# Kernel tuning notes

Hardware: AMD Instinct MI355X
Metric: run time of the kernel (lower is better)

The kernel has to match this reference:

```python
import jax, jax.numpy as jnp
import numpy as np
from jax import lax

EPS = 1e-6
DT_RANK = 24  # ceil(384/16), Mamba convention
D_STATE = 16


def _ln(x, g, b, eps=EPS):
    m = jnp.mean(x, axis=-1, keepdims=True)
    v = jnp.mean((x - m) ** 2, axis=-1, keepdims=True)
    return (x - m) * lax.rsqrt(v + eps) * g + b


def setup_inputs() -> dict:
    key = jax.random.key(0)
    ks = jax.random.split(key, 10)
    B, Dd, Hh, Ww, C = 2, 8, 16, 16, 384
    di, ds, r = 384, D_STATE, DT_RANK  # d_inner = expand * d_model = 384
    s = 0.02
    f = lambda k, shape: (jax.random.normal(k, shape, jnp.float32) * s)
    return {
        "x": jax.random.normal(ks[0], (B, Dd, Hh, Ww, C), jnp.float32),
        "g1": jnp.ones((C,), jnp.float32), "b1": jnp.zeros((C,), jnp.float32),
        "W_in": f(ks[1], (C, 2 * di)), "b_in": jnp.zeros((2 * di,), jnp.float32),
        "conv_w": f(ks[2], (di, 1, 3, 3, 3)), "conv_b": jnp.zeros((di,), jnp.float32),
        "W_x": f(ks[3], (di, r + 2 * ds)),
        "W_dt": f(ks[4], (r, di)), "b_dt": jnp.zeros((di,), jnp.float32),
        "A_log": jnp.tile(jnp.log(jnp.arange(1, ds + 1, dtype=jnp.float32)), (di, 1)),
        "D_skip": jnp.ones((di,), jnp.float32),
        "on_g": jnp.ones((di,), jnp.float32), "on_b": jnp.zeros((di,), jnp.float32),
        "W_out": f(ks[5], (di, C)), "b_out": jnp.zeros((C,), jnp.float32),
        "g2": jnp.ones((C,), jnp.float32), "b2": jnp.zeros((C,), jnp.float32),
        "W1": f(ks[6], (C, C)), "b1m": jnp.zeros((C,), jnp.float32),
        "W2": f(ks[7], (C, C)), "b2m": jnp.zeros((C,), jnp.float32),
    }


def _ss3d(h, W_in, b_in, conv_w, conv_b, W_x, W_dt, b_dt, A_log, D_skip, on_g, on_b, W_out, b_out):
    # h: [B, D, H, W, C] -> Mamba-style selective scan over flattened DHW (orientation 0)
    B, Dd, Hh, Ww, C = h.shape
    di = W_in.shape[1] // 2
    ds = D_STATE
    L = Dd * Hh * Ww
    seq = h.reshape(B, L, C)
    xz = seq @ W_in + b_in                      # [B, L, 2*di]
    xin, z = jnp.split(xz, 2, axis=-1)
    # depthwise 3D conv + SiLU on the x branch
    xc = xin.reshape(B, Dd, Hh, Ww, di).transpose(0, 4, 1, 2, 3)  # [B, di, D, H, W]
    xc = lax.conv_general_dilated(xc, conv_w, (1, 1, 1), 'SAME',
                                  feature_group_count=di,
                                  dimension_numbers=('NCDHW', 'OIDHW', 'NCDHW'))
    xc = xc + conv_b[None, :, None, None, None]
    xin = jax.nn.silu(xc).transpose(0, 2, 3, 4, 1).reshape(B, L, di)
    # input-dependent dt, B, C
    dbc = xin @ W_x                              # [B, L, r + 2*ds]
    dt, Bm, Cm = jnp.split(dbc, [DT_RANK, DT_RANK + ds], axis=-1)
    dt = jax.nn.softplus(dt @ W_dt + b_dt)       # [B, L, di]
    A = -jnp.exp(A_log)                          # [di, ds]
    dA = jnp.exp(dt[..., None] * A)              # [B, L, di, ds]
    dBx = dt[..., None] * Bm[:, :, None, :] * xin[..., None]  # [B, L, di, ds]

    def step(carry, inp):
        da, dbx, c = inp                         # [B,di,ds], [B,di,ds], [B,ds]
        carry = da * carry + dbx
        y = jnp.einsum('bds,bs->bd', carry, c)
        return carry, y

    xs = (dA.transpose(1, 0, 2, 3), dBx.transpose(1, 0, 2, 3), Cm.transpose(1, 0, 2))
    h0 = jnp.zeros((B, di, ds), dA.dtype)
    _, ys = lax.scan(step, h0, xs)               # ys: [L, B, di]
    y = ys.transpose(1, 0, 2) + xin * D_skip
    y = _ln(y, on_g, on_b) * jax.nn.silu(z)
    out = y @ W_out + b_out
    return out.reshape(B, Dd, Hh, Ww, C)


def reference(x, g1, b1, W_in, b_in, conv_w, conv_b, W_x, W_dt, b_dt, A_log, D_skip,
              on_g, on_b, W_out, b_out, g2, b2, W1, b1m, W2, b2m):
    # x + SS3D(LN(x)); then x + MLP(LN(x)).  drop_path/dropout = 0 (eval)
    a = _ss3d(_ln(x, g1, b1), W_in, b_in, conv_w, conv_b, W_x, W_dt, b_dt,
              A_log, D_skip, on_g, on_b, W_out, b_out)
    x1 = x + a
    h2 = _ln(x1, g2, b2)
    mlp = jax.nn.gelu(h2 @ W1 + b1m) @ W2 + b2m
    return x1 + mlp
```

## Files before the change

kernel.cpp:

```cpp
#include <hip/hip_runtime.h>
#include <hip/hip_bf16.h>

using bf16 = __hip_bfloat16;
#define DEV __device__ __forceinline__

typedef __attribute__((ext_vector_type(8))) short short8;
typedef __attribute__((ext_vector_type(8))) unsigned short ushort8;
typedef __attribute__((ext_vector_type(4))) float f32x4;

constexpr int Bb = 2, DD = 8, HH = 16, WW = 16;
constexpr int C = 384, DI = 384, DS = 16, RR = 24;
constexpr int L = DD * HH * WW;
constexpr int M = Bb * L;

DEV bf16 f2b(float v) { return __float2bfloat16(v); }
DEV unsigned short f2bu(float v) {
    bf16 t = __float2bfloat16(v);
    unsigned short u; __builtin_memcpy(&u, &t, 2); return u;
}
DEV float braw(unsigned short u) {
    unsigned int x = ((unsigned int)u) << 16;
    float f; __builtin_memcpy(&f, &x, 4); return f;
}

DEV float wred64(float v) {
    #pragma unroll
    for (int off = 32; off > 0; off >>= 1) v += __shfl_xor(v, off, 64);
    return v;
}
DEV float siluf(float x) { return x / (1.0f + __expf(-x)); }
DEV float softplusf(float x) { return (x > 15.0f) ? x : log1pf(__expf(x)); }
DEV float gelu_tanh(float x) {
    const float k0 = 0.7978845608028654f;
    float u = k0 * (x + 0.044715f * x * x * x);
    float e = __expf(2.0f * u);
    float t = 1.0f - 2.0f / (e + 1.0f);
    return 0.5f * x * (1.0f + t);
}

__global__ void detect_k(const unsigned short* __restrict__ g1raw,
                         int* __restrict__ flag) {
    if (threadIdx.x == 0 && blockIdx.x == 0)
        *flag = (g1raw[0] == 0x3F80) ? 1 : 0;
}

struct CvtTab {
    const void* src[17];
    float* dst[17];
    int off[18];
};
__global__ __launch_bounds__(256) void cvtmany_k(CvtTab t, const int* __restrict__ flag,
                                                 int total) {
    int i = blockIdx.x * 256 + threadIdx.x;
    if (i >= total) return;
    int seg = 0;
    #pragma unroll
    for (int k = 1; k < 18; k++) seg += (i >= t.off[k]) ? 1 : 0;
    int j = i - t.off[seg];
    const void* s = t.src[seg];
    float v = (*flag) ? __bfloat162float(((const bf16*)s)[j]) : ((const float*)s)[j];
    t.dst[seg][j] = v;
}

struct TTab {
    const void* src[4];
    unsigned short* dst[4];
    int K[4], N[4];
};
__global__ __launch_bounds__(256) void transall_k(TTab t, const int* __restrict__ flag) {
    __shared__ unsigned short tt[32][33];
    int z = blockIdx.z;
    int N = t.N[z], K = t.K[z];
    int n0 = blockIdx.x * 32, k0 = blockIdx.y * 32;
    if (n0 >= N || k0 >= K) return;
    const void* src = t.src[z];
    unsigned short* dst = t.dst[z];
    int tx = threadIdx.x & 31, ty = threadIdx.x >> 5;
    int fl = *flag;
    #pragma unroll
    for (int i = 0; i < 4; i++) {
        int k = k0 + ty + i * 8;
        unsigned short u;
        if (fl) u = ((const unsigned short*)src)[(size_t)k * N + n0 + tx];
        else    u = f2bu(((const float*)src)[(size_t)k * N + n0 + tx]);
        tt[ty + i * 8][tx] = u;
    }
    __syncthreads();
    #pragma unroll
    for (int i = 0; i < 4; i++) {
        int n = n0 + ty + i * 8;
        dst[(size_t)n * K + k0 + tx] = tt[tx][ty + i * 8];
    }
}

template <bool RAWIN>
__global__ __launch_bounds__(256) void ln_k(const void* __restrict__ xr,
                                            const float* __restrict__ g,
                                            const float* __restrict__ b,
                                            bf16* __restrict__ out,
                                            const int* __restrict__ flag) {
    bool fl = RAWIN ? (*flag != 0) : false;
    int wave = blockIdx.x * 4 + (threadIdx.x >> 6);
    int lane = threadIdx.x & 63;
    size_t base = (size_t)wave * C;
    float v[6];
    #pragma unroll
    for (int j = 0; j < 6; j++) {
        size_t idx = base + lane + 64 * j;
        if (RAWIN && fl) v[j] = braw(((const unsigned short*)xr)[idx]);
        else             v[j] = ((const float*)xr)[idx];
    }
    float s = 0.f;
    #pragma unroll
    for (int j = 0; j < 6; j++) s += v[j];
    s = wred64(s);
    float mean = s * (1.0f / C);
    float q = 0.f;
    #pragma unroll
    for (int j = 0; j < 6; j++) { float d = v[j] - mean; q += d * d; }
    q = wred64(q);
    float rstd = rsqrtf(q * (1.0f / C) + 1e-6f);
    #pragma unroll
    for (int j = 0; j < 6; j++) {
        int c = lane + 64 * j;
        out[base + c] = f2b((v[j] - mean) * rstd * g[c] + b[c]);
    }
}

enum { EPI_XZT = 0, EPI_OUT = 1, EPI_GELU = 2, EPI_FINAL = 3 };

template <int N, int EPI>
__global__ __launch_bounds__(256) void gemm_mfma(const bf16* __restrict__ A,
                                                 const unsigned short* __restrict__ Bt,
                                                 const float* __restrict__ bias,
                                                 float* __restrict__ o0,
                                                 float* __restrict__ o1,
                                                 const float* __restrict__ auxf,
                                                 const void* __restrict__ auxraw,
                                                 void* __restrict__ obf,
                                                 const int* __restrict__ flag) {
    __shared__ unsigned short Asb[128][32];
    __shared__ unsigned short Bsb[64][32];
    int tid = threadIdx.x;
    int m0 = blockIdx.x * 128, n0 = blockIdx.y * 64;
    int wid = tid >> 6, lane = tid & 63;
    int wm = wid * 32;
    int quad = lane >> 4, l15 = lane & 15;
    f32x4 acc[2][4] = {};
    int srow = tid >> 2, sseg = (tid & 3) * 8;
    const unsigned short* Au = (const unsigned short*)A;
    for (int k0 = 0; k0 < 384; k0 += 32) {
        uint4 a0 = *(const uint4*)(Au + (size_t)(m0 + srow) * 384 + k0 + sseg);
        uint4 a1 = *(const uint4*)(Au + (size_t)(m0 + 64 + srow) * 384 + k0 + sseg);
        uint4 b0 = *(const uint4*)(Bt + (size_t)(n0 + srow) * 384 + k0 + sseg);
        __syncthreads();
        *(uint4*)&Asb[srow][sseg] = a0;
        *(uint4*)&Asb[64 + srow][sseg] = a1;
        *(uint4*)&Bsb[srow][sseg] = b0;
        __syncthreads();
        short8 af[2], bfr[4];
        #pragma unroll
        for (int mt = 0; mt < 2; mt++)
            af[mt] = *(const short8*)&Asb[wm + mt * 16 + l15][quad * 8];
        #pragma unroll
        for (int nt = 0; nt < 4; nt++)
            bfr[nt] = *(const short8*)&Bsb[nt * 16 + l15][quad * 8];
        #pragma unroll
        for (int mt = 0; mt < 2; mt++)
            #pragma unroll
            for (int nt = 0; nt < 4; nt++)
                acc[mt][nt] = __builtin_amdgcn_mfma_f32_16x16x32_bf16(
                    af[mt], bfr[nt], acc[mt][nt], 0, 0, 0);
    }
    int fl = (EPI == EPI_FINAL || EPI == EPI_OUT) ? *flag : 0;
    #pragma unroll
    for (int mt = 0; mt < 2; mt++) {
        #pragma unroll
        for (int nt = 0; nt < 4; nt++) {
            int n = n0 + nt * 16 + l15;
            int mb = m0 + wm + mt * 16 + quad * 4;
            float bi = bias[n];
            if constexpr (EPI == EPI_XZT) {
                f32x4 v = acc[mt][nt];
                v[0] += bi; v[1] += bi; v[2] += bi; v[3] += bi;
                float* dst = (n < 384) ? (o0 + (size_t)n * M + mb)
                                       : (o1 + (size_t)(n - 384) * M + mb);
                *(f32x4*)dst = v;
            } else {
                #pragma unroll
                for (int r = 0; r < 4; r++) {
                    int m = mb + r;
                    float v = acc[mt][nt][r] + bi;
                    if constexpr (EPI == EPI_OUT) {
                        float av;
                        if (fl) av = braw(((const unsigned short*)auxraw)[(size_t)m * 384 + n]);
                        else    av = ((const float*)auxraw)[(size_t)m * 384 + n];
                        o0[(size_t)m * 384 + n] = v + av;
                    } else if constexpr (EPI == EPI_GELU) {
                        ((bf16*)obf)[(size_t)m * 384 + n] = f2b(gelu_tanh(v));
                    } else {
                        float rr = v + auxf[(size_t)m * 384 + n];
                        if (fl) ((bf16*)obf)[(size_t)m * 384 + n] = f2b(rr);
                        else    ((float*)obf)[(size_t)m * 384 + n] = rr;
                    }
                }
            }
        }
    }
}

__global__ __launch_bounds__(256) void convT_k(const float* __restrict__ xT,
                                               const float* __restrict__ cw,
                                               const float* __restrict__ cb,
                                               float* __restrict__ xinT) {
    int c = blockIdx.y;
    int m = blockIdx.x * 256 + threadIdx.x;
    int l = m & (L - 1);
    int d = l >> 8, h = (l >> 4) & 15, w = l & 15;
    const float* xc = xT + (size_t)c * M;
    float acc = cb[c];
    #pragma unroll
    for (int kd = -1; kd <= 1; kd++) {
        int dd = d + kd; if ((unsigned)dd >= 8u) continue;
        #pragma unroll
        for (int kh = -1; kh <= 1; kh++) {
            int hh = h + kh; if ((unsigned)hh >= 16u) continue;
            #pragma unroll
            for (int kw = -1; kw <= 1; kw++) {
                int ww = w + kw; if ((unsigned)ww >= 16u) continue;
                acc = fmaf(xc[m + kd * 256 + kh * 16 + kw],
                           cw[c * 27 + (kd + 1) * 9 + (kh + 1) * 3 + (kw + 1)], acc);
            }
        }
    }
    xinT[(size_t)c * M + m] = siluf(acc);
}

__global__ __launch_bounds__(256) void dbc2_k(const float* __restrict__ xinT,
                                              const float* __restrict__ Wx,
                                              float* __restrict__ part) {
    __shared__ float As[16][64];
    __shared__ float Ws[16 * 56];
    int tid = threadIdx.x;
    int m0 = blockIdx.x * 64;
    int kc = blockIdx.y;
    int tm = tid & 63, grp = tid >> 6;
    int kk = tid >> 4, mc = (tid & 15) * 4;
    float acc[14] = {};
    for (int k0 = kc * 64; k0 < kc * 64 + 64; k0 += 16) {
        float4 av = *(const float4*)(xinT + (size_t)(k0 + kk) * M + m0 + mc);
        __syncthreads();
        *(float4*)&As[kk][mc] = av;
        for (int idx = tid; idx < 16 * 56; idx += 256)
            Ws[idx] = Wx[k0 * 56 + idx];
        __syncthreads();
        #pragma unroll
        for (int k = 0; k < 16; k++) {
            float a = As[k][tm];
            #pragma unroll
            for (int jj = 0; jj < 14; jj++)
                acc[jj] = fmaf(a, Ws[k * 56 + grp * 14 + jj], acc[jj]);
        }
    }
    int m = m0 + tm;
    #pragma unroll
    for (int jj = 0; jj < 14; jj++) {
        int col = grp * 14 + jj;
        part[((size_t)kc * 56 + col) * M + m] = acc[jj];
    }
}

__global__ __launch_bounds__(256) void dbcred_k(const float* __restrict__ part,
                                                float* __restrict__ dtrT,
                                                unsigned short* __restrict__ Brow,
                                                unsigned short* __restrict__ Crow) {
    int col = blockIdx.y;
    int m = blockIdx.x * 256 + threadIdx.x;
    float s = 0.f;
    #pragma unroll
    for (int kc = 0; kc < 6; kc++)
        s += part[((size_t)kc * 56 + col) * M + m];
    if (col < 24)      dtrT[(size_t)col * M + m] = s;
    else if (col < 40) Brow[(size_t)m * 16 + col - 24] = f2bu(s);
    else               Crow[(size_t)m * 16 + col - 40] = f2bu(s);
}

__global__ __launch_bounds__(256) void dtT_k(const float* __restrict__ dtrT,
                                             const float* __restrict__ Wdt,
                                             const float* __restrict__ bdt,
                                             float* __restrict__ dtT) {
    int lane = threadIdx.x & 63;
    int wv = threadIdx.x >> 6;
    int n = blockIdx.y * 4 + wv;
    int m = blockIdx.x * 64 + lane;
    float acc = bdt[n];
    #pragma unroll
    for (int j = 0; j < 24; j++)
        acc = fmaf(dtrT[(size_t)j * M + m], Wdt[j * 384 + n], acc);
    dtT[(size_t)n * M + m] = softplusf(acc);
}

__global__ __launch_bounds__(128) void scan4_k(const float* __restrict__ dtT,
                                               const float* __restrict__ xinT,
                                               const unsigned short* __restrict__ Brow,
                                               const unsigned short* __restrict__ Crow,
                                               const float* __restrict__ alog,
                                               const float* __restrict__ dsk,
                                               float* __restrict__ yT) {
    __shared__ float dt_s[2112], x_s[2112];
    __shared__ float ypart[2 * 2112];
    int bi = blockIdx.x;
    int b = bi / DI, d = bi % DI;
    int wave = threadIdx.x >> 6, lane = threadIdx.x & 63;
    int s0 = wave * 8;
    float Aneg[8];
    #pragma unroll
    for (int ss = 0; ss < 8; ss++) Aneg[ss] = -__expf(alog[d * DS + s0 + ss]);
    const float* dtp = dtT + (size_t)d * M + b * L;
    const float* xp  = xinT + (size_t)d * M + b * L;
    #pragma unroll
    for (int i = 0; i < 4; i++) {
        int t4 = (threadIdx.x + i * 128) * 4;
        float4 dv = *(const float4*)(dtp + t4);
        float4 xv = *(const float4*)(xp + t4);
        int base = t4 + (t4 >> 5);
        dt_s[base + 0] = dv.x; dt_s[base + 1] = dv.y;
        dt_s[base + 2] = dv.z; dt_s[base + 3] = dv.w;
        x_s[base + 0] = xv.x; x_s[base + 1] = xv.y;
        x_s[base + 2] = xv.z; x_s[base + 3] = xv.w;
    }
    __syncthreads();
    const unsigned short* Bp = Brow + ((size_t)b * L) * 16 + s0;
    const unsigned short* Cp = Crow + ((size_t)b * L) * 16 + s0;
    int tbase = lane * 32;
    int pbase = lane * 33;
    float Ap[8], Bg[8];
    #pragma unroll
    for (int ss = 0; ss < 8; ss++) { Ap[ss] = 1.f; Bg[ss] = 0.f; }
    #pragma unroll 4
    for (int j = 0; j < 32; j++) {
        float dtv = dt_s[pbase + j];
        float dxv = dtv * x_s[pbase + j];
        ushort8 bu = *(const ushort8*)(Bp + (size_t)(tbase + j) * 16);
        #pragma unroll
        for (int ss = 0; ss < 8; ss++) {
            float dA = __expf(dtv * Aneg[ss]);
            Bg[ss] = fmaf(dA, Bg[ss], dxv * braw(bu[ss]));
            Ap[ss] *= dA;
        }
    }
    float carry[8];
    #pragma unroll
    for (int ss = 0; ss < 8; ss++) {
        float a = Ap[ss], bb = Bg[ss];
        #pragma unroll
        for (int off = 1; off < 64; off <<= 1) {
            float ap = __shfl_up(a, off, 64);
            float bp = __shfl_up(bb, off, 64);
            if (lane >= off) { bb = fmaf(a, bp, bb); a *= ap; }
        }
        float c = __shfl_up(bb, 1, 64);
        carry[ss] = (lane == 0) ? 0.f : c;
    }
    float* ypw = ypart + wave * 2112;
    float h[8];
    #pragma unroll
    for (int ss = 0; ss < 8; ss++) h[ss] = carry[ss];
    #pragma unroll 4
    for (int j = 0; j < 32; j++) {
        float dtv = dt_s[pbase + j];
        float dxv = dtv * x_s[pbase + j];
        size_t toff = (size_t)(tbase + j) * 16;
        ushort8 bu = *(const ushort8*)(Bp + toff);
        ushort8 cu = *(const ushort8*)(Cp + toff);
        float acc = 0.f;
        #pragma unroll
        for (int ss = 0; ss < 8; ss++) {
            float dA = __expf(dtv * Aneg[ss]);
            h[ss] = fmaf(dA, h[ss], dxv * braw(bu[ss]));
            acc = fmaf(h[ss], braw(cu[ss]), acc);
        }
        ypw[pbase + j] = acc;
    }
    __syncthreads();
    float Dv = dsk[d];
    float* yp = yT + (size_t)d * M + b * L;
    #pragma unroll
    for (int i = 0; i < 16; i++) {
        int t = threadIdx.x + 128 * i;
        int ti = t + (t >> 5);
        yp[t] = fmaf(x_s[ti], Dv, ypart[ti] + ypart[2112 + ti]);
    }
}

__global__ __launch_bounds__(256) void lnmulT_k(const float* __restrict__ yT,
                                                const float* __restrict__ zT,
                                                const float* __restrict__ g,
                                                const float* __restrict__ b,
                                                unsigned short* __restrict__ yact) {
    __shared__ float rs1[8][32], rs2[8][32];
    __shared__ float meanb[32], rstdb[32];
    __shared__ unsigned short tile[32][392];
    int moff = threadIdx.x & 31;
    int dsub = threadIdx.x >> 5;
    int m0 = blockIdx.x * 32;
    size_t mg = m0 + moff;
    float s1 = 0.f, s2 = 0.f;
    #pragma unroll 8
    for (int j = 0; j < 48; j++) {
        int d = dsub + 8 * j;
        float v = yT[(size_t)d * M + mg];
        s1 += v; s2 += v * v;
    }
    rs1[dsub][moff] = s1;
    rs2[dsub][moff] = s2;
    __syncthreads();
    if (threadIdx.x < 32) {
        float a1 = 0.f, a2 = 0.f;
        #pragma unroll
        for (int ss = 0; ss < 8; ss++) { a1 += rs1[ss][threadIdx.x]; a2 += rs2[ss][threadIdx.x]; }
        float mean = a1 * (1.0f / DI);
        float var = a2 * (1.0f / DI) - mean * mean;
        meanb[threadIdx.x] = mean;
        rstdb[threadIdx.x] = rsqrtf(var + 1e-6f);
    }
    __syncthreads();
    float mean = meanb[moff], rstd = rstdb[moff];
    #pragma unroll 8
    for (int j = 0; j < 48; j++) {
        int d = dsub + 8 * j;
        float v = yT[(size_t)d * M + mg];
        float ln = (v - mean) * rstd * g[d] + b[d];
        float zv = zT[(size_t)d * M + mg];
        tile[moff][d] = f2bu(ln * siluf(zv));
    }
    __syncthreads();
    #pragma unroll
    for (int i = 0; i < 6; i++) {
        int chunk = threadIdx.x + 256 * i;
        int row = chunk / 48, cc = chunk % 48;
        *(uint4*)(yact + ((size_t)(m0 + row)) * 384 + cc * 8) =
            *(const uint4*)&tile[row][cc * 8];
    }
}

extern "C" void kernel_launch(void* const* d_in, const int* in_sizes, int n_in,
                              void* d_out, int out_size, void* d_ws, size_t ws_size,
                              hipStream_t stream) {
    float* ws = (float*)d_ws;
    constexpr size_t S = (size_t)M * 384;
    bf16*  hb   = (bf16*)ws;
    float* xT   = ws + S / 2;
    float* zT   = xT + S;
    float* xinT = zT + S;
    float* dtT  = xinT + S;
    float* x1   = dtT + S;
    float* dtrT = x1 + S;
    unsigned short* Brow = (unsigned short*)(dtrT + (size_t)24 * M);
    unsigned short* Crow = Brow + (size_t)M * 16;
    float* part = (float*)(Crow + (size_t)M * 16);
    float* smalls = part + (size_t)6 * 56 * M;

    float* g1f  = smalls;        float* b1f  = g1f + 384;
    float* binf = b1f + 384;     float* cwf  = binf + 768;
    float* cbf  = cwf + 10368;   float* wxf  = cbf + 384;
    float* wdtf = wxf + 21504;   float* bdtf = wdtf + 9216;
    float* alogf= bdtf + 384;    float* dskf = alogf + 6144;
    float* ongf = dskf + 384;    float* onbf = ongf + 384;
    float* boutf= onbf + 384;    float* g2f  = boutf + 384;
    float* b2f_ = g2f + 384;     float* b1mf = b2f_ + 384;
    float* b2mf = b1mf + 384;
    unsigned short* WinT  = (unsigned short*)(b2mf + 384);
    unsigned short* WoutT = WinT + 294912;
    unsigned short* W1T   = WoutT + 147456;
    unsigned short* W2T   = W1T + 147456;
    int* flag = (int*)(W2T + 147456);

    float* yT = xT;
    bf16* h2b = hb;
    unsigned short* yactb = (unsigned short*)dtT;
    unsigned short* m1b = (unsigned short*)zT;

    detect_k<<<1, 64, 0, stream>>>((const unsigned short*)d_in[1], flag);

    CvtTab tab;
    {
        int idxs[17] = {1, 2, 4, 5, 6, 7, 8, 9, 10, 11, 12, 13, 15, 16, 17, 19, 21};
        float* dsts[17] = {g1f, b1f, binf, cwf, cbf, wxf, wdtf, bdtf, alogf, dskf,
                           ongf, onbf, boutf, g2f, b2f_, b1mf, b2mf};
        int ns[17] = {384, 384, 768, 10368, 384, 21504, 9216, 384, 6144, 384,
                      384, 384, 384, 384, 384, 384, 384};
        int off = 0;
        for (int k = 0; k < 17; k++) {
            tab.src[k] = d_in[idxs[k]];
            tab.dst[k] = dsts[k];
            tab.off[k] = off;
            off += ns[k];
        }
        tab.off[17] = off;
        cvtmany_k<<<(off + 255) / 256, 256, 0, stream>>>(tab, flag, off);
    }
    {
        TTab tt;
        tt.src[0] = d_in[3];  tt.dst[0] = WinT;  tt.K[0] = 384; tt.N[0] = 768;
        tt.src[1] = d_in[14]; tt.dst[1] = WoutT; tt.K[1] = 384; tt.N[1] = 384;
        tt.src[2] = d_in[18]; tt.dst[2] = W1T;   tt.K[2] = 384; tt.N[2] = 384;
        tt.src[3] = d_in[20]; tt.dst[3] = W2T;   tt.K[3] = 384; tt.N[3] = 384;
        transall_k<<<dim3(24, 12, 4), 256, 0, stream>>>(tt, flag);
    }

    ln_k<true><<<M / 4, 256, 0, stream>>>(d_in[0], g1f, b1f, hb, flag);
    gemm_mfma<768, EPI_XZT><<<dim3(M / 128, 12), 256, 0, stream>>>(
        hb, WinT, binf, xT, zT, nullptr, nullptr, nullptr, flag);
    convT_k<<<dim3(M / 256, DI), 256, 0, stream>>>(xT, cwf, cbf, xinT);
    dbc2_k<<<dim3(M / 64, 6), 256, 0, stream>>>(xinT, wxf, part);
    dbcred_k<<<dim3(M / 256, 56), 256, 0, stream>>>(part, dtrT, Brow, Crow);
    dtT_k<<<dim3(M / 64, DI / 4), 256, 0, stream>>>(dtrT, wdtf, bdtf, dtT);
    scan4_k<<<Bb * DI, 128, 0, stream>>>(dtT, xinT, Brow, Crow, alogf, dskf, yT);
    lnmulT_k<<<M / 32, 256, 0, stream>>>(yT, zT, ongf, onbf, yactb);
    gemm_mfma<384, EPI_OUT><<<dim3(M / 128, 6), 256, 0, stream>>>(
        (const bf16*)yactb, WoutT, boutf, x1, nullptr, nullptr, d_in[0], nullptr, flag);
    ln_k<false><<<M / 4, 256, 0, stream>>>(x1, g2f, b2f_, h2b, flag);
    gemm_mfma<384, EPI_GELU><<<dim3(M / 128, 6), 256, 0, stream>>>(
        h2b, W1T, b1mf, nullptr, nullptr, nullptr, nullptr, m1b, flag);
    gemm_mfma<384, EPI_FINAL><<<dim3(M / 128, 6), 256, 0, stream>>>(
        (const bf16*)m1b, W2T, b2mf, nullptr, nullptr, x1, nullptr, d_out, flag);
}
```

Baseline: 244.7 us.

## Merge prep kernels, use direct global-to-LDS loads, widen in-proj GEMM tile, vectorize conv

Removes the flag-detect kernel and merges the weight conversion and transpose kernels into one prep launch, with each kernel reading the dtype marker from g1 directly. The GEMM now stages tiles with global_load_lds instead of register round-trips, and the in-projection uses a 128x128 tile so each wave computes more output. The depthwise conv computes four outputs per thread with float4 loads and stores, reusing neighbouring values. These changes cut launch count and memory traffic, at the cost of a second barrier-free LDS path that depends on correct async load ordering and higher register use in the wide tile.

```diff
diff --git a/kernel.cpp b/kernel.cpp
--- a/kernel.cpp
+++ b/kernel.cpp
@@ -21,6 +21,13 @@
 DEV float braw(unsigned short u) {
     unsigned int x = ((unsigned int)u) << 16;
     float f; __builtin_memcpy(&f, &x, 4); return f;
+}
+DEV bool isbf(const unsigned short* g1p) { return g1p[0] == 0x3F80; }
+
+typedef const __attribute__((address_space(1))) unsigned int* gaddr_t;
+typedef __attribute__((address_space(3))) unsigned int* laddr_t;
+DEV void gload_lds16(const void* g, void* l) {
+    __builtin_amdgcn_global_load_lds((gaddr_t)g, (laddr_t)l, 16, 0, 0);
 }
 
 DEV float wred64(float v) {
@@ -38,58 +45,51 @@
     return 0.5f * x * (1.0f + t);
 }
 
-__global__ void detect_k(const unsigned short* __restrict__ g1raw,
-                         int* __restrict__ flag) {
-    if (threadIdx.x == 0 && blockIdx.x == 0)
-        *flag = (g1raw[0] == 0x3F80) ? 1 : 0;
-}
-
-struct CvtTab {
-    const void* src[17];
-    float* dst[17];
-    int off[18];
+struct PrepTab {
+    const void* tsrc[4];
+    unsigned short* tdst[4];
+    int tK[4], tN[4];
+    const void* csrc[17];
+    float* cdst[17];
+    int coff[18];
 };
-__global__ __launch_bounds__(256) void cvtmany_k(CvtTab t, const int* __restrict__ flag,
-                                                 int total) {
-    int i = blockIdx.x * 256 + threadIdx.x;
-    if (i >= total) return;
-    int seg = 0;
-    #pragma unroll
-    for (int k = 1; k < 18; k++) seg += (i >= t.off[k]) ? 1 : 0;
-    int j = i - t.off[seg];
-    const void* s = t.src[seg];
-    float v = (*flag) ? __bfloat162float(((const bf16*)s)[j]) : ((const float*)s)[j];
-    t.dst[seg][j] = v;
-}
-
-struct TTab {
-    const void* src[4];
-    unsigned short* dst[4];
-    int K[4], N[4];
-};
-__global__ __launch_bounds__(256) void transall_k(TTab t, const int* __restrict__ flag) {
-    __shared__ unsigned short tt[32][33];
+__global__ __launch_bounds__(256) void prep_k(PrepTab t,
+                                              const unsigned short* __restrict__ g1p,
+                                              int ctotal) {
+    bool fl = isbf(g1p);
     int z = blockIdx.z;
-    int N = t.N[z], K = t.K[z];
-    int n0 = blockIdx.x * 32, k0 = blockIdx.y * 32;
-    if (n0 >= N || k0 >= K) return;
-    const void* src = t.src[z];
-    unsigned short* dst = t.dst[z];
-    int tx = threadIdx.x & 31, ty = threadIdx.x >> 5;
-    int fl = *flag;
-    #pragma unroll
-    for (int i = 0; i < 4; i++) {
-        int k = k0 + ty + i * 8;
-        unsigned short u;
-        if (fl) u = ((const unsigned short*)src)[(size_t)k * N + n0 + tx];
-        else    u = f2bu(((const float*)src)[(size_t)k * N + n0 + tx]);
-        tt[ty + i * 8][tx] = u;
-    }
-    __syncthreads();
-    #pragma unroll
-    for (int i = 0; i < 4; i++) {
-        int n = n0 + ty + i * 8;
-        dst[(size_t)n * K + k0 + tx] = tt[tx][ty + i * 8];
+    if (z < 4) {
+        __shared__ unsigned short tt[32][33];
+        int N = t.tN[z], K = t.tK[z];
+        int n0 = blockIdx.x * 32, k0 = blockIdx.y * 32;
+        if (n0 >= N || k0 >= K) return;
+        const void* src = t.tsrc[z];
+        unsigned short* dst = t.tdst[z];
+        int tx = threadIdx.x & 31, ty = threadIdx.x >> 5;
+        #pragma unroll
+        for (int i = 0; i < 4; i++) {
+            int k = k0 + ty + i * 8;
+            unsigned short u;
+            if (fl) u = ((const unsigned short*)src)[(size_t)k * N + n0 + tx];
+            else    u = f2bu(((const float*)src)[(size_t)k * N + n0 + tx]);
+            tt[ty + i * 8][tx] = u;
+        }
+        __syncthreads();
+        #pragma unroll
+        for (int i = 0; i < 4; i++) {
+            int n = n0 + ty + i * 8;
+            dst[(size_t)n * K + k0 + tx] = tt[tx][ty + i * 8];
+        }
+    } else {
+        int i = (blockIdx.y * 24 + blockIdx.x) * 256 + threadIdx.x;
+        if (i >= ctotal) return;
+        int seg = 0;
+        #pragma unroll
+        for (int k = 1; k < 18; k++) seg += (i >= t.coff[k]) ? 1 : 0;
+        int j = i - t.coff[seg];
+        const void* s = t.csrc[seg];
+        float v = fl ? braw(((const unsigned short*)s)[j]) : ((const float*)s)[j];
+        t.cdst[seg][j] = v;
     }
 }
 
@@ -98,8 +98,8 @@
                                             const float* __restrict__ g,
                                             const float* __restrict__ b,
                                             bf16* __restrict__ out,
-                                            const int* __restrict__ flag) {
-    bool fl = RAWIN ? (*flag != 0) : false;
+                                            const unsigned short* __restrict__ g1p) {
+    bool fl = RAWIN ? isbf(g1p) : false;
     int wave = blockIdx.x * 4 + (threadIdx.x >> 6);
     int lane = threadIdx.x & 63;
     size_t base = (size_t)wave * C;
@@ -129,7 +129,7 @@
 
 enum { EPI_XZT = 0, EPI_OUT = 1, EPI_GELU = 2, EPI_FINAL = 3 };
 
-template <int N, int EPI>
+template <int N, int TN, int EPI>
 __global__ __launch_bounds__(256) void gemm_mfma(const bf16* __restrict__ A,
                                                  const unsigned short* __restrict__ Bt,
                                                  const float* __restrict__ bias,
@@ -138,46 +138,51 @@
                                                  const float* __restrict__ auxf,
                                                  const void* __restrict__ auxraw,
                                                  void* __restrict__ obf,
-                                                 const int* __restrict__ flag) {
-    __shared__ unsigned short Asb[128][32];
-    __shared__ unsigned short Bsb[64][32];
+                                                 const unsigned short* __restrict__ g1p) {
+    __shared__ unsigned short Asb[128 * 32];
+    __shared__ unsigned short Bsb[TN * 32];
+    constexpr int MT = (TN == 128) ? 4 : 2;
     int tid = threadIdx.x;
-    int m0 = blockIdx.x * 128, n0 = blockIdx.y * 64;
+    int m0 = blockIdx.x * 128, n0 = blockIdx.y * TN;
     int wid = tid >> 6, lane = tid & 63;
-    int wm = wid * 32;
+    int wm = (TN == 128) ? (wid >> 1) * 64 : wid * 32;
+    int wn = (TN == 128) ? (wid & 1) * 64 : 0;
     int quad = lane >> 4, l15 = lane & 15;
-    f32x4 acc[2][4] = {};
+    f32x4 acc[MT][4] = {};
     int srow = tid >> 2, sseg = (tid & 3) * 8;
     const unsigned short* Au = (const unsigned short*)A;
     for (int k0 = 0; k0 < 384; k0 += 32) {
-        uint4 a0 = *(const uint4*)(Au + (size_t)(m0 + srow) * 384 + k0 + sseg);
-        uint4 a1 = *(const uint4*)(Au + (size_t)(m0 + 64 + srow) * 384 + k0 + sseg);
-        uint4 b0 = *(const uint4*)(Bt + (size_t)(n0 + srow) * 384 + k0 + sseg);
         __syncthreads();
-        *(uint4*)&Asb[srow][sseg] = a0;
-        *(uint4*)&Asb[64 + srow][sseg] = a1;
-        *(uint4*)&Bsb[srow][sseg] = b0;
+        gload_lds16(Au + (size_t)(m0 + srow) * 384 + k0 + sseg,
+                    &Asb[srow * 32 + sseg]);
+        gload_lds16(Au + (size_t)(m0 + 64 + srow) * 384 + k0 + sseg,
+                    &Asb[(64 + srow) * 32 + sseg]);
+        gload_lds16(Bt + (size_t)(n0 + srow) * 384 + k0 + sseg,
+                    &Bsb[srow * 32 + sseg]);
+        if constexpr (TN == 128)
+            gload_lds16(Bt + (size_t)(n0 + 64 + srow) * 384 + k0 + sseg,
+                        &Bsb[(64 + srow) * 32 + sseg]);
         __syncthreads();
-        short8 af[2], bfr[4];
-        #pragma unroll
-        for (int mt = 0; mt < 2; mt++)
-            af[mt] = *(const short8*)&Asb[wm + mt * 16 + l15][quad * 8];
+        short8 af[MT], bfr[4];
+        #pragma unroll
+        for (int mt = 0; mt < MT; mt++)
+            af[mt] = *(const short8*)&Asb[(wm + mt * 16 + l15) * 32 + quad * 8];
         #pragma unroll
         for (int nt = 0; nt < 4; nt++)
-            bfr[nt] = *(const short8*)&Bsb[nt * 16 + l15][quad * 8];
-        #pragma unroll
-        for (int mt = 0; mt < 2; mt++)
+            bfr[nt] = *(const short8*)&Bsb[(wn + nt * 16 + l15) * 32 + quad * 8];
+        #pragma unroll
+        for (int mt = 0; mt < MT; mt++)
             #pragma unroll
             for (int nt = 0; nt < 4; nt++)
                 acc[mt][nt] = __builtin_amdgcn_mfma_f32_16x16x32_bf16(
                     af[mt], bfr[nt], acc[mt][nt], 0, 0, 0);
     }
-    int fl = (EPI == EPI_FINAL || EPI == EPI_OUT) ? *flag : 0;
-    #pragma unroll
-    for (int mt = 0; mt < 2; mt++) {
+    bool fl = (EPI == EPI_FINAL || EPI == EPI_OUT) ? isbf(g1p) : false;
+    #pragma unroll
+    for (int mt = 0; mt < MT; mt++) {
         #pragma unroll
         for (int nt = 0; nt < 4; nt++) {
-            int n = n0 + nt * 16 + l15;
+            int n = n0 + wn + nt * 16 + l15;
             int mb = m0 + wm + mt * 16 + quad * 4;
             float bi = bias[n];
             if constexpr (EPI == EPI_XZT) {
@@ -214,26 +219,34 @@
                                                const float* __restrict__ cb,
                                                float* __restrict__ xinT) {
     int c = blockIdx.y;
-    int m = blockIdx.x * 256 + threadIdx.x;
-    int l = m & (L - 1);
-    int d = l >> 8, h = (l >> 4) & 15, w = l & 15;
+    int m0 = (blockIdx.x * 256 + threadIdx.x) * 4;
+    int l = m0 & (L - 1);
+    int d = l >> 8, h = (l >> 4) & 15, w0 = l & 15;
     const float* xc = xT + (size_t)c * M;
-    float acc = cb[c];
+    const float* wc = cw + c * 27;
+    float bias = cb[c];
+    float acc[4] = {bias, bias, bias, bias};
     #pragma unroll
     for (int kd = -1; kd <= 1; kd++) {
         int dd = d + kd; if ((unsigned)dd >= 8u) continue;
         #pragma unroll
         for (int kh = -1; kh <= 1; kh++) {
             int hh = h + kh; if ((unsigned)hh >= 16u) continue;
+            int mm = m0 + kd * 256 + kh * 16;
+            float vv[6];
+            vv[0] = (w0 == 0) ? 0.f : xc[mm - 1];
+            float4 v14 = *(const float4*)(xc + mm);
+            vv[1] = v14.x; vv[2] = v14.y; vv[3] = v14.z; vv[4] = v14.w;
+            vv[5] = (w0 == 12) ? 0.f : xc[mm + 4];
+            const float* wk = wc + (kd + 1) * 9 + (kh + 1) * 3;
+            float wa = wk[0], wb = wk[1], wcc = wk[2];
             #pragma unroll
-            for (int kw = -1; kw <= 1; kw++) {
-                int ww = w + kw; if ((unsigned)ww >= 16u) continue;
-                acc = fmaf(xc[m + kd * 256 + kh * 16 + kw],
-                           cw[c * 27 + (kd + 1) * 9 + (kh + 1) * 3 + (kw + 1)], acc);
-            }
-        }
-    }
-    xinT[(size_t)c * M + m] = siluf(acc);
+            for (int j = 0; j < 4; j++)
+                acc[j] = fmaf(vv[j], wa, fmaf(vv[j + 1], wb, fmaf(vv[j + 2], wcc, acc[j])));
+        }
+    }
+    float4 o = make_float4(siluf(acc[0]), siluf(acc[1]), siluf(acc[2]), siluf(acc[3]));
+    *(float4*)(xinT + (size_t)c * M + m0) = o;
 }
 
 __global__ __launch_bounds__(256) void dbc2_k(const float* __restrict__ xinT,
@@ -474,17 +487,19 @@
     unsigned short* WoutT = WinT + 294912;
     unsigned short* W1T   = WoutT + 147456;
     unsigned short* W2T   = W1T + 147456;
-    int* flag = (int*)(W2T + 147456);
 
     float* yT = xT;
     bf16* h2b = hb;
     unsigned short* yactb = (unsigned short*)dtT;
     unsigned short* m1b = (unsigned short*)zT;
-
-    detect_k<<<1, 64, 0, stream>>>((const unsigned short*)d_in[1], flag);
-
-    CvtTab tab;
+    const unsigned short* g1p = (const unsigned short*)d_in[1];
+
+    PrepTab tab;
     {
+        tab.tsrc[0] = d_in[3];  tab.tdst[0] = WinT;  tab.tK[0] = 384; tab.tN[0] = 768;
+        tab.tsrc[1] = d_in[14]; tab.tdst[1] = WoutT; tab.tK[1] = 384; tab.tN[1] = 384;
+        tab.tsrc[2] = d_in[18]; tab.tdst[2] = W1T;   tab.tK[2] = 384; tab.tN[2] = 384;
+        tab.tsrc[3] = d_in[20]; tab.tdst[3] = W2T;   tab.tK[3] = 384; tab.tN[3] = 384;
         int idxs[17] = {1, 2, 4, 5, 6, 7, 8, 9, 10, 11, 12, 13, 15, 16, 17, 19, 21};
         float* dsts[17] = {g1f, b1f, binf, cwf, cbf, wxf, wdtf, bdtf, alogf, dskf,
                            ongf, onbf, boutf, g2f, b2f_, b1mf, b2mf};
@@ -492,37 +507,29 @@
                       384, 384, 384, 384, 384, 384, 384};
         int off = 0;
         for (int k = 0; k < 17; k++) {
-            tab.src[k] = d_in[idxs[k]];
-            tab.dst[k] = dsts[k];
-            tab.off[k] = off;
+            tab.csrc[k] = d_in[idxs[k]];
+            tab.cdst[k] = dsts[k];
+            tab.coff[k] = off;
             off += ns[k];
         }
-        tab.off[17] = off;
-        cvtmany_k<<<(off + 255) / 256, 256, 0, stream>>>(tab, flag, off);
-    }
-    {
-        TTab tt;
-        tt.src[0] = d_in[3];  tt.dst[0] = WinT;  tt.K[0] = 384; tt.N[0] = 768;
-        tt.src[1] = d_in[14]; tt.dst[1] = WoutT; tt.K[1] = 384; tt.N[1] = 384;
-        tt.src[2] = d_in[18]; tt.dst[2] = W1T;   tt.K[2] = 384; tt.N[2] = 384;
-        tt.src[3] = d_in[20]; tt.dst[3] = W2T;   tt.K[3] = 384; tt.N[3] = 384;
-        transall_k<<<dim3(24, 12, 4), 256, 0, stream>>>(tt, flag);
-    }
-
-    ln_k<true><<<M / 4, 256, 0, stream>>>(d_in[0], g1f, b1f, hb, flag);
-    gemm_mfma<768, EPI_XZT><<<dim3(M / 128, 12), 256, 0, stream>>>(
-        hb, WinT, binf, xT, zT, nullptr, nullptr, nullptr, flag);
-    convT_k<<<dim3(M / 256, DI), 256, 0, stream>>>(xT, cwf, cbf, xinT);
+        tab.coff[17] = off;
+        prep_k<<<dim3(24, 12, 5), 256, 0, stream>>>(tab, g1p, off);
+    }
+
+    ln_k<true><<<M / 4, 256, 0, stream>>>(d_in[0], g1f, b1f, hb, g1p);
+    gemm_mfma<768, 128, EPI_XZT><<<dim3(M / 128, 6), 256, 0, stream>>>(
+        hb, WinT, binf, xT, zT, nullptr, nullptr, nullptr, g1p);
+    convT_k<<<dim3(M / 1024, DI), 256, 0, stream>>>(xT, cwf, cbf, xinT);
     dbc2_k<<<dim3(M / 64, 6), 256, 0, stream>>>(xinT, wxf, part);
     dbcred_k<<<dim3(M / 256, 56), 256, 0, stream>>>(part, dtrT, Brow, Crow);
     dtT_k<<<dim3(M / 64, DI / 4), 256, 0, stream>>>(dtrT, wdtf, bdtf, dtT);
     scan4_k<<<Bb * DI, 128, 0, stream>>>(dtT, xinT, Brow, Crow, alogf, dskf, yT);
     lnmulT_k<<<M / 32, 256, 0, stream>>>(yT, zT, ongf, onbf, yactb);
-    gemm_mfma<384, EPI_OUT><<<dim3(M / 128, 6), 256, 0, stream>>>(
-        (const bf16*)yactb, WoutT, boutf, x1, nullptr, nullptr, d_in[0], nullptr, flag);
-    ln_k<false><<<M / 4, 256, 0, stream>>>(x1, g2f, b2f_, h2b, flag);
-    gemm_mfma<384, EPI_GELU><<<dim3(M / 128, 6), 256, 0, stream>>>(
-        h2b, W1T, b1mf, nullptr, nullptr, nullptr, nullptr, m1b, flag);
-    gemm_mfma<384, EPI_FINAL><<<dim3(M / 128, 6), 256, 0, stream>>>(
-        (const bf16*)m1b, W2T, b2mf, nullptr, nullptr, x1, nullptr, d_out, flag);
-}
+    gemm_mfma<384, 64, EPI_OUT><<<dim3(M / 128, 6), 256, 0, stream>>>(
+        (const bf16*)yactb, WoutT, boutf, x1, nullptr, nullptr, d_in[0], nullptr, g1p);
+    ln_k<false><<<M / 4, 256, 0, stream>>>(x1, g2f, b2f_, h2b, g1p);
+    gemm_mfma<384, 64, EPI_GELU><<<dim3(M / 128, 6), 256, 0, stream>>>(
+        h2b, W1T, b1mf, nullptr, nullptr, nullptr, nullptr, m1b, g1p);
+    gemm_mfma<384, 64, EPI_FINAL><<<dim3(M / 128, 6), 256, 0, stream>>>(
+        (const bf16*)m1b, W2T, b2mf, nullptr, nullptr, x1, nullptr, d_out, g1p);
+}
```

Result: faster. 230.6 us (-5.8%).
